# Kernel optimization log

Hardware: AMD Instinct MI355X
Metric: run time of the kernel (lower is better)

The kernel has to match this reference:

```python
import jax, jax.numpy as jnp
import numpy as np

HEAD_COUNT = 6  # module scales by head_count**-0.5, not head_size
SCALE = HEAD_COUNT ** (-0.5)


def setup_inputs() -> dict:
    key = jax.random.key(0)
    kx, kq, kk, kv = jax.random.split(key, 4)
    B, T, C, H = 512, 128, 384, 64
    x = jax.random.normal(kx, (B, T, C), dtype=jnp.float32)
    init = (1.0 / np.sqrt(C)).astype(np.float32)
    Wq = jax.random.normal(kq, (C, H), dtype=jnp.float32) * init
    Wk = jax.random.normal(kk, (C, H), dtype=jnp.float32) * init
    Wv = jax.random.normal(kv, (C, H), dtype=jnp.float32) * init
    return {"x": x, "Wq": Wq, "Wk": Wk, "Wv": Wv}


def reference(x, Wq, Wk, Wv):
    # x: [B, T, C]; Wq/Wk/Wv: [C, H]
    q = jnp.einsum('btc,ch->bth', x, Wq)
    k = jnp.einsum('btc,ch->bth', x, Wk)
    v = jnp.einsum('btc,ch->bth', x, Wv)
    # scores: [B, T, T], scaled by head_count**-0.5 (faithful to source)
    scores = jnp.einsum('bth,bsh->bts', q, k) * SCALE
    T = x.shape[1]
    causal = jnp.tril(jnp.ones((T, T), dtype=bool))
    scores = jnp.where(causal, scores, -jnp.inf)
    weights = jax.nn.softmax(scores, axis=-1)
    # dropout omitted (eval mode / identity for reference baseline)
    return jnp.einsum('bts,bsh->bth', weights, v)
```

## Files before the change

### kernel.cpp

```cpp
#include <hip/hip_runtime.h>
#include <hip/hip_bf16.h>


#define B_ 512
#define T_ 128
#define C_ 384
#define H_ 64

typedef __bf16 bf16;
typedef __attribute__((ext_vector_type(8))) __bf16 bf16x8;
typedef __attribute__((ext_vector_type(4))) __bf16 bf16x4;
typedef __attribute__((ext_vector_type(4))) float f32x4;

__global__ void build_wt(const float* __restrict__ Wq, const float* __restrict__ Wk,
                         const float* __restrict__ Wv, bf16* __restrict__ Wt)
{
    int t = blockIdx.x * 256 + threadIdx.x;
    if (t >= 12 * 12 * 64) return;
    int lane = t & 63;
    int tn   = (t >> 6) % 12;
    int kc   = t / (12 * 64);
    int lm = lane & 15, quad = lane >> 4;
    int n = tn * 16 + lm;
    int j = n >> 6, h = n & 63;
    const float* Wp = (j == 0) ? Wq : (j == 1) ? Wk : Wv;
    int k0 = kc * 32 + quad * 8;
    bf16x8 v;
#pragma unroll
    for (int e = 0; e < 8; ++e) v[e] = (bf16)Wp[(k0 + e) * H_ + h];
    *(bf16x8*)&Wt[t * 8] = v;
}


__launch_bounds__(512, 4)
__global__ void head_fused(const float* __restrict__ x,
                           const bf16* __restrict__ Wt,
                           float* __restrict__ out)
{
    __shared__ bf16 lds[24576];
    bf16* Qs  = lds;
    bf16* Ks  = lds + 8192;
    bf16* Vts = lds + 16384;
    bf16* Ps  = lds;

    const int tid  = threadIdx.x;
    const int w    = tid >> 6;
    const int lane = tid & 63;
    const int lm   = lane & 15;
    const int quad = lane >> 4;
    const int mg   = w >> 2;
    const int ng   = w & 3;
    const int b    = blockIdx.x;

    const float* xb = x + (size_t)b * (T_ * C_);

    f32x4 acc[4][3];
#pragma unroll
    for (int mf = 0; mf < 4; ++mf)
#pragma unroll
        for (int nf = 0; nf < 3; ++nf) acc[mf][nf] = (f32x4){0.f, 0.f, 0.f, 0.f};

    const float* xr   = xb + (size_t)(64 * mg + lm) * C_ + quad * 8;
    const bf16*  wbase = Wt + (size_t)(3 * ng) * 512 + lane * 8;

    float4 buf[8];
    auto LD = [&](int kc) {
#pragma unroll
        for (int mf = 0; mf < 4; ++mf) {
            const float4* p = (const float4*)(xr + mf * 16 * C_ + kc * 32);
            buf[2 * mf]     = p[0];
            buf[2 * mf + 1] = p[1];
        }
    };

    LD(0);
#pragma unroll
    for (int kc = 0; kc < 12; ++kc) {
        bf16x8 afr[4];
#pragma unroll
        for (int mf = 0; mf < 4; ++mf) {
            float4 p0 = buf[2 * mf], p1 = buf[2 * mf + 1];
            afr[mf] = (bf16x8){(bf16)p0.x, (bf16)p0.y, (bf16)p0.z, (bf16)p0.w,
                               (bf16)p1.x, (bf16)p1.y, (bf16)p1.z, (bf16)p1.w};
        }
        if (kc < 11) LD(kc + 1);
#pragma unroll
        for (int nf = 0; nf < 3; ++nf) {
            bf16x8 bfr = *(const bf16x8*)(wbase + (size_t)kc * 6144 + nf * 512);
#pragma unroll
            for (int mf = 0; mf < 4; ++mf)
                acc[mf][nf] =
                    __builtin_amdgcn_mfma_f32_16x16x32_bf16(afr[mf], bfr, acc[mf][nf], 0, 0, 0);
        }
    }

#pragma unroll
    for (int mf = 0; mf < 4; ++mf) {
#pragma unroll
        for (int nf = 0; nf < 3; ++nf) {
            int tn = 3 * ng + nf;
            int gn = 16 * tn + lm;
            int j = gn >> 6, h = gn & 63;
            int m0 = 64 * mg + 16 * mf + quad * 4;
            if (j == 2) {
                bf16x4 v4 = {(bf16)acc[mf][nf][0], (bf16)acc[mf][nf][1],
                             (bf16)acc[mf][nf][2], (bf16)acc[mf][nf][3]};
                int pc = (m0 & 7) | ((((m0 >> 3) ^ (h & 15)) & 15) << 3);
                *(bf16x4*)&Vts[h * 128 + pc] = v4;
            } else {
                bf16* dst = (j == 0) ? Qs : Ks;
#pragma unroll
                for (int r = 0; r < 4; ++r) {
                    int m = m0 + r;
                    int pc = (h & 7) | ((((h >> 3) ^ (m & 7)) & 7) << 3);
                    dst[m * 64 + pc] = (bf16)acc[mf][nf][r];
                }
            }
        }
    }
    __syncthreads();

    const float SCALE = 0.40824829046386307f;
    const int tm = w;
    const int mrow = 16 * tm + lm;

    f32x4 sacc[8];
#pragma unroll
    for (int t = 0; t < 8; ++t) sacc[t] = (f32x4){0.f, 0.f, 0.f, 0.f};

    bf16x8 qa[2];
#pragma unroll
    for (int ks = 0; ks < 2; ++ks) {
        int phys = ((ks * 4 + quad) ^ (mrow & 7)) & 7;
        qa[ks] = *(const bf16x8*)&Qs[mrow * 64 + phys * 8];
    }
#pragma unroll
    for (int tn = 0; tn < 8; ++tn) {
        if (tn <= tm) {
            int nrow = 16 * tn + lm;
#pragma unroll
            for (int ks = 0; ks < 2; ++ks) {
                int phys = ((ks * 4 + quad) ^ (nrow & 7)) & 7;
                bf16x8 kb = *(const bf16x8*)&Ks[nrow * 64 + phys * 8];
                sacc[tn] =
                    __builtin_amdgcn_mfma_f32_16x16x32_bf16(qa[ks], kb, sacc[tn], 0, 0, 0);
            }
        }
    }

#pragma unroll
    for (int r = 0; r < 4; ++r) {
        int m = 16 * tm + quad * 4 + r;
        float mx = -1e30f;
#pragma unroll
        for (int tn = 0; tn < 8; ++tn) {
            if (tn <= tm) {
                int n = 16 * tn + lm;
                float v = (n <= m) ? sacc[tn][r] * SCALE : -1e30f;
                sacc[tn][r] = v;
                mx = fmaxf(mx, v);
            }
        }
#pragma unroll
        for (int off = 1; off < 16; off <<= 1) mx = fmaxf(mx, __shfl_xor(mx, off, 16));
        float sum = 0.f;
#pragma unroll
        for (int tn = 0; tn < 8; ++tn) {
            if (tn <= tm) {
                float e = __expf(sacc[tn][r] - mx);
                sacc[tn][r] = e;
                sum += e;
            }
        }
#pragma unroll
        for (int off = 1; off < 16; off <<= 1) sum += __shfl_xor(sum, off, 16);
        float inv = 1.f / sum;
#pragma unroll
        for (int tn = 0; tn < 8; ++tn) {
            if (tn <= tm) sacc[tn][r] *= inv;
        }
    }

    __syncthreads();

#pragma unroll
    for (int tn = 0; tn < 8; ++tn) {
        if (tn <= tm) {
            int n = 16 * tn + lm;
#pragma unroll
            for (int r = 0; r < 4; ++r) {
                int m = 16 * tm + quad * 4 + r;
                int pc = (n & 7) | ((((n >> 3) ^ (m & 15)) & 15) << 3);
                Ps[m * 128 + pc] = (bf16)sacc[tn][r];
            }
        }
    }
    if ((tm & 1) == 0) {
        int m = 16 * tm + lm;
        int c0 = 16 * (tm + 1) + quad * 4;
        int pc = (c0 & 7) | ((((c0 >> 3) ^ (m & 15)) & 15) << 3);
        *(bf16x4*)&Ps[m * 128 + pc] =
            (bf16x4){(bf16)0.f, (bf16)0.f, (bf16)0.f, (bf16)0.f};
    }

    f32x4 oacc[4];
#pragma unroll
    for (int t = 0; t < 4; ++t) oacc[t] = (f32x4){0.f, 0.f, 0.f, 0.f};

    const int nks = (tm + 2) >> 1;
    for (int ks = 0; ks < nks; ++ks) {
        int unit = ks * 4 + quad;
        int phys = (unit ^ (mrow & 15)) & 15;
        bf16x8 pa = *(const bf16x8*)&Ps[mrow * 128 + phys * 8];
#pragma unroll
        for (int th = 0; th < 4; ++th) {
            int hrow = 16 * th + lm;
            int ph2 = (unit ^ (hrow & 15)) & 15;
            bf16x8 vb = *(const bf16x8*)&Vts[hrow * 128 + ph2 * 8];
            oacc[th] =
                __builtin_amdgcn_mfma_f32_16x16x32_bf16(pa, vb, oacc[th], 0, 0, 0);
        }
    }

    float* ob = out + (size_t)b * (T_ * H_);
#pragma unroll
    for (int th = 0; th < 4; ++th) {
        int h = 16 * th + lm;
#pragma unroll
        for (int r = 0; r < 4; ++r) {
            int m = 16 * tm + quad * 4 + r;
            ob[m * 64 + h] = oacc[th][r];
        }
    }
}

extern "C" void kernel_launch(void* const* d_in, const int* in_sizes, int n_in,
                              void* d_out, int out_size, void* d_ws, size_t ws_size,
                              hipStream_t stream) {
    const float* x  = (const float*)d_in[0];
    const float* Wq = (const float*)d_in[1];
    const float* Wk = (const float*)d_in[2];
    const float* Wv = (const float*)d_in[3];
    float* o = (float*)d_out;
    bf16* Wt = (bf16*)d_ws;
    build_wt<<<dim3(36), dim3(256), 0, stream>>>(Wq, Wk, Wv, Wt);
    head_fused<<<dim3(B_), dim3(512), 0, stream>>>(x, Wt, o);
}
```

Baseline: 191.0 us.

## Stage x tiles into LDS via async global_load_lds triple buffering

```diff
diff --git a/kernel.cpp b/kernel.cpp
--- a/kernel.cpp
+++ b/kernel.cpp
@@ -11,6 +11,11 @@
 typedef __attribute__((ext_vector_type(8))) __bf16 bf16x8;
 typedef __attribute__((ext_vector_type(4))) __bf16 bf16x4;
 typedef __attribute__((ext_vector_type(4))) float f32x4;
+
+#define GLOAD_LDS16(g, l)                                                     \
+    __builtin_amdgcn_global_load_lds(                                         \
+        (const __attribute__((address_space(1))) void*)(g),                   \
+        (__attribute__((address_space(3))) void*)(l), 16, 0, 0)
 
 __global__ void build_wt(const float* __restrict__ Wq, const float* __restrict__ Wk,
                          const float* __restrict__ Wv, bf16* __restrict__ Wt)
@@ -37,11 +42,12 @@
                            const bf16* __restrict__ Wt,
                            float* __restrict__ out)
 {
-    __shared__ bf16 lds[24576];
+    __shared__ __align__(16) bf16 lds[24576];
     bf16* Qs  = lds;
     bf16* Ks  = lds + 8192;
     bf16* Vts = lds + 16384;
     bf16* Ps  = lds;
+    float* xstage = (float*)lds;
 
     const int tid  = threadIdx.x;
     const int w    = tid >> 6;
@@ -60,30 +66,42 @@
 #pragma unroll
         for (int nf = 0; nf < 3; ++nf) acc[mf][nf] = (f32x4){0.f, 0.f, 0.f, 0.f};
 
-    const float* xr   = xb + (size_t)(64 * mg + lm) * C_ + quad * 8;
-    const bf16*  wbase = Wt + (size_t)(3 * ng) * 512 + lane * 8;
-
-    float4 buf[8];
-    auto LD = [&](int kc) {
+    const bf16* wbase = Wt + (size_t)(3 * ng) * 512 + lane * 8;
+
+    const int u0row = tid >> 3, u0unit = tid & 7;
+    const int u1row = (tid + 512) >> 3, u1unit = tid & 7;
+    const float* g0 = xb + (size_t)u0row * C_ + (u0unit ^ (u0row & 7)) * 4;
+    const float* g1 = xb + (size_t)u1row * C_ + (u1unit ^ (u1row & 7)) * 4;
+    char* l0 = (char*)lds + (size_t)(w * 64) * 16;
+    char* l1 = (char*)lds + (size_t)(512 + w * 64) * 16;
+
+    auto STAGE = [&](int kc) {
+        int bo = (kc % 3) * 16384;
+        GLOAD_LDS16(g0 + kc * 32, l0 + bo);
+        GLOAD_LDS16(g1 + kc * 32, l1 + bo);
+    };
+
+    STAGE(0);
+    STAGE(1);
+    asm volatile("s_waitcnt vmcnt(2)" ::: "memory");
+    __builtin_amdgcn_s_barrier();
+
+#pragma unroll
+    for (int kc = 0; kc < 12; ++kc) {
+        if (kc + 2 < 12) STAGE(kc + 2);
+
+        const float* xc = xstage + (kc % 3) * 4096;
+        bf16x8 afr[4];
 #pragma unroll
         for (int mf = 0; mf < 4; ++mf) {
-            const float4* p = (const float4*)(xr + mf * 16 * C_ + kc * 32);
-            buf[2 * mf]     = p[0];
-            buf[2 * mf + 1] = p[1];
-        }
-    };
-
-    LD(0);
-#pragma unroll
-    for (int kc = 0; kc < 12; ++kc) {
-        bf16x8 afr[4];
-#pragma unroll
-        for (int mf = 0; mf < 4; ++mf) {
-            float4 p0 = buf[2 * mf], p1 = buf[2 * mf + 1];
-            afr[mf] = (bf16x8){(bf16)p0.x, (bf16)p0.y, (bf16)p0.z, (bf16)p0.w,
-                               (bf16)p1.x, (bf16)p1.y, (bf16)p1.z, (bf16)p1.w};
-        }
-        if (kc < 11) LD(kc + 1);
+            int row = 64 * mg + 16 * mf + lm;
+            int p0 = (2 * quad) ^ (row & 7);
+            int p1 = (2 * quad + 1) ^ (row & 7);
+            f32x4 va = *(const f32x4*)(xc + row * 32 + p0 * 4);
+            f32x4 vb = *(const f32x4*)(xc + row * 32 + p1 * 4);
+            afr[mf] = (bf16x8){(bf16)va[0], (bf16)va[1], (bf16)va[2], (bf16)va[3],
+                               (bf16)vb[0], (bf16)vb[1], (bf16)vb[2], (bf16)vb[3]};
+        }
 #pragma unroll
         for (int nf = 0; nf < 3; ++nf) {
             bf16x8 bfr = *(const bf16x8*)(wbase + (size_t)kc * 6144 + nf * 512);
@@ -92,7 +110,14 @@
                 acc[mf][nf] =
                     __builtin_amdgcn_mfma_f32_16x16x32_bf16(afr[mf], bfr, acc[mf][nf], 0, 0, 0);
         }
-    }
+
+        if (kc < 11) {
+            if (kc < 10) asm volatile("s_waitcnt vmcnt(2)" ::: "memory");
+            else         asm volatile("s_waitcnt vmcnt(0)" ::: "memory");
+            __builtin_amdgcn_s_barrier();
+        }
+    }
+    __syncthreads();
 
 #pragma unroll
     for (int mf = 0; mf < 4; ++mf) {
```

After: 171.1 us. 1.12x faster.

## Stage x tile through LDS with fully coalesced loads and prefetch weights

Applied to the files above, without the earlier changes.

```diff
diff --git a/kernel.cpp b/kernel.cpp
--- a/kernel.cpp
+++ b/kernel.cpp
@@ -32,12 +32,12 @@
 }
 
 
-__launch_bounds__(512, 4)
+__launch_bounds__(512, 2)
 __global__ void head_fused(const float* __restrict__ x,
                            const bf16* __restrict__ Wt,
                            float* __restrict__ out)
 {
-    __shared__ bf16 lds[24576];
+    __shared__ __align__(16) bf16 lds[49152];
     bf16* Qs  = lds;
     bf16* Ks  = lds + 8192;
     bf16* Vts = lds + 16384;
@@ -52,7 +52,31 @@
     const int ng   = w & 3;
     const int b    = blockIdx.x;
 
-    const float* xb = x + (size_t)b * (T_ * C_);
+    const float4* xb4 = (const float4*)(x + (size_t)b * (T_ * C_));
+    float4 xv[24];
+#pragma unroll
+    for (int j = 0; j < 24; ++j) xv[j] = xb4[tid * 24 + j];
+
+    const bf16* wl = Wt + (size_t)(3 * ng) * 512 + lane * 8;
+    bf16x8 wc0 = *(const bf16x8*)(wl);
+    bf16x8 wc1 = *(const bf16x8*)(wl + 512);
+    bf16x8 wc2 = *(const bf16x8*)(wl + 1024);
+
+    {
+        const int row = tid >> 2;
+        const int u0  = (tid & 3) * 12;
+#pragma unroll
+        for (int jp = 0; jp < 12; ++jp) {
+            float4 a = xv[2 * jp], c = xv[2 * jp + 1];
+            bf16x8 v = {(bf16)a.x, (bf16)a.y, (bf16)a.z, (bf16)a.w,
+                        (bf16)c.x, (bf16)c.y, (bf16)c.z, (bf16)c.w};
+            int u16  = u0 + jp;
+            int phys = (u16 & ~7) | ((u16 ^ row) & 7);
+            *(bf16x8*)&lds[row * 384 + phys * 8] = v;
+        }
+    }
+    asm volatile("s_waitcnt lgkmcnt(0)" ::: "memory");
+    __builtin_amdgcn_s_barrier();
 
     f32x4 acc[4][3];
 #pragma unroll
@@ -60,39 +84,32 @@
 #pragma unroll
         for (int nf = 0; nf < 3; ++nf) acc[mf][nf] = (f32x4){0.f, 0.f, 0.f, 0.f};
 
-    const float* xr   = xb + (size_t)(64 * mg + lm) * C_ + quad * 8;
-    const bf16*  wbase = Wt + (size_t)(3 * ng) * 512 + lane * 8;
-
-    float4 buf[8];
-    auto LD = [&](int kc) {
+#pragma unroll
+    for (int kc = 0; kc < 12; ++kc) {
+        bf16x8 wn0 = wc0, wn1 = wc1, wn2 = wc2;
+        if (kc < 11) {
+            const bf16* wp = wl + (size_t)(kc + 1) * 6144;
+            wn0 = *(const bf16x8*)(wp);
+            wn1 = *(const bf16x8*)(wp + 512);
+            wn2 = *(const bf16x8*)(wp + 1024);
+        }
+        bf16x8 afr[4];
 #pragma unroll
         for (int mf = 0; mf < 4; ++mf) {
-            const float4* p = (const float4*)(xr + mf * 16 * C_ + kc * 32);
-            buf[2 * mf]     = p[0];
-            buf[2 * mf + 1] = p[1];
-        }
-    };
-
-    LD(0);
-#pragma unroll
-    for (int kc = 0; kc < 12; ++kc) {
-        bf16x8 afr[4];
+            int row  = 64 * mg + 16 * mf + lm;
+            int u16  = kc * 4 + quad;
+            int phys = (u16 & ~7) | ((u16 ^ row) & 7);
+            afr[mf] = *(const bf16x8*)&lds[row * 384 + phys * 8];
+        }
 #pragma unroll
         for (int mf = 0; mf < 4; ++mf) {
-            float4 p0 = buf[2 * mf], p1 = buf[2 * mf + 1];
-            afr[mf] = (bf16x8){(bf16)p0.x, (bf16)p0.y, (bf16)p0.z, (bf16)p0.w,
-                               (bf16)p1.x, (bf16)p1.y, (bf16)p1.z, (bf16)p1.w};
-        }
-        if (kc < 11) LD(kc + 1);
-#pragma unroll
-        for (int nf = 0; nf < 3; ++nf) {
-            bf16x8 bfr = *(const bf16x8*)(wbase + (size_t)kc * 6144 + nf * 512);
-#pragma unroll
-            for (int mf = 0; mf < 4; ++mf)
-                acc[mf][nf] =
-                    __builtin_amdgcn_mfma_f32_16x16x32_bf16(afr[mf], bfr, acc[mf][nf], 0, 0, 0);
-        }
-    }
+            acc[mf][0] = __builtin_amdgcn_mfma_f32_16x16x32_bf16(afr[mf], wc0, acc[mf][0], 0, 0, 0);
+            acc[mf][1] = __builtin_amdgcn_mfma_f32_16x16x32_bf16(afr[mf], wc1, acc[mf][1], 0, 0, 0);
+            acc[mf][2] = __builtin_amdgcn_mfma_f32_16x16x32_bf16(afr[mf], wc2, acc[mf][2], 0, 0, 0);
+        }
+        wc0 = wn0; wc1 = wn1; wc2 = wn2;
+    }
+    __syncthreads();
 
 #pragma unroll
     for (int mf = 0; mf < 4; ++mf) {
```

Result: faster. 178.7 us (-6.5%).
